# Kernel tuning notes

Measured on AMD Instinct MI355X. Metric: run time of the kernel, lower is better.

Reference implementation:

```python
import jax, jax.numpy as jnp
import numpy as np

B, LQ, LK, D = 8, 2048, 2048, 128
NEG = -100000.0


def setup_inputs() -> dict:
    key = jax.random.key(0)
    kq, kk, kv, km = jax.random.split(key, 4)
    q = jax.random.normal(kq, (B, LQ, D), dtype=jnp.float32)
    k = jax.random.normal(kk, (B, LK, D), dtype=jnp.float32)
    v = jax.random.normal(kv, (B, LK, D), dtype=jnp.float32)
    mask = jax.random.randint(km, (B, LQ, LK), 0, 2, dtype=jnp.int32)
    return {"q": q, "k": k, "v": v, "mask": mask}


def reference(q, k, v, mask):
    # atten_score = q @ k^T / sqrt(d)   [B, Lq, Lk]
    scores = jnp.einsum("bqd,bkd->bqk", q, k) / jnp.sqrt(jnp.float32(q.shape[-1]))
    # mask_mod == 2: additive mask, masked positions pushed to large negative
    scores = scores + mask.astype(jnp.float32) * NEG
    # sigmoid instead of softmax (no normalization across keys)
    attn = jax.nn.sigmoid(scores)
    return jnp.einsum("bqk,bkd->bqd", attn, v)
```

## Files before the change

kernel.cpp:

```cpp
#include <hip/hip_runtime.h>
#include <hip/hip_bf16.h>

#define B_   8
#define LQ_  2048
#define LK_  2048
#define D_   128
#define QBLK 64
#define KBLK 64
#define NT   (LK_ / KBLK)
#define THREADS 512
#define SCALE 0.08838834764831845f

typedef __attribute__((ext_vector_type(8))) __bf16 bf16x8;
typedef __attribute__((ext_vector_type(4))) __bf16 bf16x4;
typedef __attribute__((ext_vector_type(4))) float  f32x4;
typedef __attribute__((ext_vector_type(4))) float  fx4;

#define QS_OFF 0
#define KS_OFF 8704
#define VT_OFF 17408
#define PS_OFF 26624
#define SMEM_ELEMS 31744

__global__ __launch_bounds__(THREADS, 2)
void sigattn_kernel(const float* __restrict__ q, const float* __restrict__ k,
                    const float* __restrict__ v, const int* __restrict__ mask,
                    float* __restrict__ out)
{
    __shared__ __bf16 smem[SMEM_ELEMS];

    const int tid  = threadIdx.x;
    const int lane = tid & 63;
    const int wid  = tid >> 6;
    const int qg   = wid & 3;
    const int kg   = wid >> 2;
    const int l15  = lane & 15;
    const int g    = lane >> 4;

    const int bid   = blockIdx.x;
    const int b     = bid & 7;
    const int q0    = (bid >> 3) * QBLK;

    const float* qb = q + (size_t)b * LQ_ * D_ + (size_t)q0 * D_;
    const float* kb = k + (size_t)b * LK_ * D_;
    const float* vb = v + (size_t)b * LK_ * D_;
    const int*   mb = mask + (size_t)b * LQ_ * LK_ + (size_t)q0 * LK_;
    float*       ob = out + (size_t)b * LQ_ * D_ + (size_t)q0 * D_;

    __bf16* Qs = smem + QS_OFF;
    __bf16* Ks = smem + KS_OFF;
    __bf16* Vt = smem + VT_OFF;
    __bf16* Ps = smem + PS_OFF + wid * 640;

    const int dv  = tid & 127;
    const int kq8 = tid >> 7;

    int mcur[8];

#pragma unroll
    for (int i = 0; i < 4; ++i) {
        int idx = tid + i * THREADS;
        int row = idx >> 5, c4 = idx & 31;
        fx4 f = *(const fx4*)(qb + row * D_ + c4 * 4);
        bf16x4 w; w[0]=(__bf16)f[0]; w[1]=(__bf16)f[1]; w[2]=(__bf16)f[2]; w[3]=(__bf16)f[3];
        *(bf16x4*)(Qs + row * 136 + c4 * 4) = w;
    }
#pragma unroll
    for (int i = 0; i < 4; ++i) {
        int idx = tid + i * THREADS;
        int row = idx >> 5, c4 = idx & 31;
        fx4 f = *(const fx4*)(kb + row * D_ + c4 * 4);
        bf16x4 w; w[0]=(__bf16)f[0]; w[1]=(__bf16)f[1]; w[2]=(__bf16)f[2]; w[3]=(__bf16)f[3];
        *(bf16x4*)(Ks + row * 136 + c4 * 4) = w;
    }
#pragma unroll
    for (int i = 0; i < 4; ++i) {
        int quad = kq8 + i * 4;
        bf16x4 w;
#pragma unroll
        for (int j = 0; j < 4; ++j) w[j] = (__bf16)vb[(quad * 4 + j) * D_ + dv];
        *(bf16x4*)(Vt + dv * 72 + quad * 4) = w;
    }
#pragma unroll
    for (int n2 = 0; n2 < 2; ++n2)
#pragma unroll
        for (int r = 0; r < 4; ++r)
            mcur[n2 * 4 + r] = mb[(qg * 16 + 4 * g + r) * LK_ + (kg * 32 + n2 * 16 + l15)];

    __syncthreads();

    bf16x8 qfrag[4];
#pragma unroll
    for (int dblk = 0; dblk < 4; ++dblk)
        qfrag[dblk] = *(const bf16x8*)(Qs + (qg * 16 + l15) * 136 + dblk * 32 + g * 8);

    f32x4 oacc[8];
#pragma unroll
    for (int nb = 0; nb < 8; ++nb) oacc[nb] = (f32x4){0.f, 0.f, 0.f, 0.f};

    for (int t = 0; t < NT; ++t) {
        const bool more = (t + 1 < NT);

        fx4   kreg[4];
        float vreg[16];
        int   mnxt[8];
        if (more) {
            const int kt = (t + 1) * KBLK;
#pragma unroll
            for (int i = 0; i < 4; ++i) {
                int idx = tid + i * THREADS;
                int row = idx >> 5, c4 = idx & 31;
                kreg[i] = *(const fx4*)(kb + (kt + row) * D_ + c4 * 4);
            }
#pragma unroll
            for (int i = 0; i < 4; ++i) {
                int quad = kq8 + i * 4;
#pragma unroll
                for (int j = 0; j < 4; ++j)
                    vreg[i * 4 + j] = vb[(kt + quad * 4 + j) * D_ + dv];
            }
#pragma unroll
            for (int n2 = 0; n2 < 2; ++n2)
#pragma unroll
                for (int r = 0; r < 4; ++r)
                    mnxt[n2 * 4 + r] = mb[(qg * 16 + 4 * g + r) * LK_ + (kt + kg * 32 + n2 * 16 + l15)];
        }

        f32x4 sacc[2];
        sacc[0] = (f32x4){0.f, 0.f, 0.f, 0.f};
        sacc[1] = (f32x4){0.f, 0.f, 0.f, 0.f};
#pragma unroll
        for (int n2 = 0; n2 < 2; ++n2) {
            const __bf16* krow = Ks + (kg * 32 + n2 * 16 + l15) * 136 + g * 8;
#pragma unroll
            for (int dblk = 0; dblk < 4; ++dblk) {
                bf16x8 bfr = *(const bf16x8*)(krow + dblk * 32);
                sacc[n2] = __builtin_amdgcn_mfma_f32_16x16x32_bf16(qfrag[dblk], bfr, sacc[n2], 0, 0, 0);
            }
        }

#pragma unroll
        for (int n2 = 0; n2 < 2; ++n2)
#pragma unroll
            for (int r = 0; r < 4; ++r) {
                float s = sacc[n2][r] * SCALE;
                float p = (mcur[n2 * 4 + r] != 0) ? 0.0f : 1.0f / (1.0f + __expf(-s));
                Ps[(4 * g + r) * 40 + n2 * 16 + l15] = (__bf16)p;
            }

        bf16x8 pfrag = *(const bf16x8*)(Ps + l15 * 40 + g * 8);
#pragma unroll
        for (int nb = 0; nb < 8; ++nb) {
            bf16x8 vfr = *(const bf16x8*)(Vt + (nb * 16 + l15) * 72 + kg * 32 + g * 8);
            oacc[nb] = __builtin_amdgcn_mfma_f32_16x16x32_bf16(pfrag, vfr, oacc[nb], 0, 0, 0);
        }

        __syncthreads();

        if (more) {
#pragma unroll
            for (int i = 0; i < 4; ++i) {
                int idx = tid + i * THREADS;
                int row = idx >> 5, c4 = idx & 31;
                bf16x4 w;
                w[0]=(__bf16)kreg[i][0]; w[1]=(__bf16)kreg[i][1];
                w[2]=(__bf16)kreg[i][2]; w[3]=(__bf16)kreg[i][3];
                *(bf16x4*)(Ks + row * 136 + c4 * 4) = w;
            }
#pragma unroll
            for (int i = 0; i < 4; ++i) {
                int quad = kq8 + i * 4;
                bf16x4 w;
#pragma unroll
                for (int j = 0; j < 4; ++j) w[j] = (__bf16)vreg[i * 4 + j];
                *(bf16x4*)(Vt + dv * 72 + quad * 4) = w;
            }
#pragma unroll
            for (int j = 0; j < 8; ++j) mcur[j] = mnxt[j];
        }

        __syncthreads();
    }

    float* red = (float*)smem;
    if (kg == 0) {
#pragma unroll
        for (int nb = 0; nb < 8; ++nb)
#pragma unroll
            for (int r = 0; r < 4; ++r)
                red[(qg * 16 + 4 * g + r) * 132 + nb * 16 + l15] = oacc[nb][r];
    }
    __syncthreads();
    if (kg == 1) {
#pragma unroll
        for (int nb = 0; nb < 8; ++nb)
#pragma unroll
            for (int r = 0; r < 4; ++r) {
                int row = qg * 16 + 4 * g + r;
                float val = red[row * 132 + nb * 16 + l15] + oacc[nb][r];
                ob[(size_t)row * D_ + nb * 16 + l15] = val;
            }
    }
}

extern "C" void kernel_launch(void* const* d_in, const int* in_sizes, int n_in,
                              void* d_out, int out_size, void* d_ws, size_t ws_size,
                              hipStream_t stream) {
    const float* q    = (const float*)d_in[0];
    const float* k    = (const float*)d_in[1];
    const float* v    = (const float*)d_in[2];
    const int*   mask = (const int*)d_in[3];
    float*       out  = (float*)d_out;

    dim3 grid(B_ * (LQ_ / QBLK));
    dim3 block(THREADS);
    sigattn_kernel<<<grid, block, 0, stream>>>(q, k, v, mask, out);
}
```

Baseline: 237.6 us.

## Precast K/V to bf16 in prep kernels and stream fragments directly from global

Adds two pre-kernels that convert K to bf16 and transpose V to bf16 in a permuted layout in the workspace. The main kernel now loads its MFMA fragments straight from global memory (L2-resident) instead of staging through LDS, which removes the per-tile barriers. Warps are regrouped into 2 query groups × 2 key slices × 2 key-tile parities, each warp covering 32 query rows. The mask is read with vectorized nontemporal loads, and the sigmoid uses exp2 plus a hardware reciprocal. The cost is two extra launches, more redundant global and L2 traffic per warp, and a four-stage serialized reduction at the end.

```diff
diff --git a/kernel.cpp b/kernel.cpp
--- a/kernel.cpp
+++ b/kernel.cpp
@@ -7,199 +7,220 @@
 #define D_   128
 #define QBLK 64
 #define KBLK 64
-#define NT   (LK_ / KBLK)
 #define THREADS 512
 #define SCALE 0.08838834764831845f
+#define NEGL2E (-1.44269504088896340736f * SCALE)
 
 typedef __attribute__((ext_vector_type(8))) __bf16 bf16x8;
-typedef __attribute__((ext_vector_type(4))) __bf16 bf16x4;
 typedef __attribute__((ext_vector_type(4))) float  f32x4;
 typedef __attribute__((ext_vector_type(4))) float  fx4;
-
-#define QS_OFF 0
-#define KS_OFF 8704
-#define VT_OFF 17408
-#define PS_OFF 26624
-#define SMEM_ELEMS 31744
+typedef __attribute__((ext_vector_type(4))) int    i32x4;
+
+__global__ __launch_bounds__(256)
+void kprep(const float* __restrict__ k, __bf16* __restrict__ kb)
+{
+    size_t i = ((size_t)blockIdx.x * 256 + threadIdx.x) * 8;
+    fx4 a = *(const fx4*)(k + i);
+    fx4 b = *(const fx4*)(k + i + 4);
+    bf16x8 w;
+#pragma unroll
+    for (int j = 0; j < 4; ++j) { w[j] = (__bf16)a[j]; w[4 + j] = (__bf16)b[j]; }
+    *(bf16x8*)(kb + i) = w;
+}
+
+__global__ __launch_bounds__(128)
+void vprep(const float* __restrict__ v, __bf16* __restrict__ vt)
+{
+    const int b  = blockIdx.x & 7;
+    const int k0 = (blockIdx.x >> 3) * 64;
+    const int d  = threadIdx.x;
+    const float* vb = v + ((size_t)b * LK_ + k0) * D_ + d;
+    __bf16* vr = vt + ((size_t)b * D_ + d) * LK_ + k0;
+#pragma unroll
+    for (int grp = 0; grp < 2; ++grp) {
+#pragma unroll
+        for (int g = 0; g < 4; ++g) {
+            bf16x8 w;
+#pragma unroll
+            for (int e = 0; e < 8; ++e) {
+                int h = e >> 2, j = e & 3;
+                int key = grp * 32 + h * 16 + g * 4 + j;
+                w[e] = (__bf16)vb[(size_t)key * D_];
+            }
+            *(bf16x8*)(vr + grp * 32 + g * 8) = w;
+        }
+    }
+}
 
 __global__ __launch_bounds__(THREADS, 2)
-void sigattn_kernel(const float* __restrict__ q, const float* __restrict__ k,
-                    const float* __restrict__ v, const int* __restrict__ mask,
-                    float* __restrict__ out)
+void sigattn_main(const float* __restrict__ q, const int* __restrict__ mask,
+                  const __bf16* __restrict__ Kb, const __bf16* __restrict__ Vt,
+                  float* __restrict__ out)
 {
-    __shared__ __bf16 smem[SMEM_ELEMS];
+    __shared__ float red[64 * 132];
 
     const int tid  = threadIdx.x;
     const int lane = tid & 63;
-    const int wid  = tid >> 6;
-    const int qg   = wid & 3;
-    const int kg   = wid >> 2;
     const int l15  = lane & 15;
     const int g    = lane >> 4;
+    const int wid  = tid >> 6;
+    const int qg   = wid & 1;
+    const int kg   = (wid >> 1) & 1;
+    const int tp   = wid >> 2;
 
     const int bid   = blockIdx.x;
     const int b     = bid & 7;
     const int q0    = (bid >> 3) * QBLK;
-
-    const float* qb = q + (size_t)b * LQ_ * D_ + (size_t)q0 * D_;
-    const float* kb = k + (size_t)b * LK_ * D_;
-    const float* vb = v + (size_t)b * LK_ * D_;
-    const int*   mb = mask + (size_t)b * LQ_ * LK_ + (size_t)q0 * LK_;
-    float*       ob = out + (size_t)b * LQ_ * D_ + (size_t)q0 * D_;
-
-    __bf16* Qs = smem + QS_OFF;
-    __bf16* Ks = smem + KS_OFF;
-    __bf16* Vt = smem + VT_OFF;
-    __bf16* Ps = smem + PS_OFF + wid * 640;
-
-    const int dv  = tid & 127;
-    const int kq8 = tid >> 7;
-
-    int mcur[8];
-
-#pragma unroll
-    for (int i = 0; i < 4; ++i) {
-        int idx = tid + i * THREADS;
+    const int qbase = qg * 32;
+
+    const float*  qb = q    + ((size_t)b * LQ_ + q0) * D_;
+    const int*    mb = mask + ((size_t)b * LQ_ + q0) * LK_;
+    const __bf16* kb = Kb   + (size_t)b * LK_ * D_;
+    const __bf16* vt = Vt   + (size_t)b * D_ * LK_;
+    float*        ob = out  + ((size_t)b * LQ_ + q0) * D_;
+
+    bf16x8 qfrag[2][4];
+#pragma unroll
+    for (int qq = 0; qq < 2; ++qq) {
+        const float* qrow = qb + (size_t)(qbase + qq * 16 + l15) * D_;
+#pragma unroll
+        for (int dblk = 0; dblk < 4; ++dblk) {
+            fx4 f0 = *(const fx4*)(qrow + dblk * 32 + g * 8);
+            fx4 f1 = *(const fx4*)(qrow + dblk * 32 + g * 8 + 4);
+            bf16x8 w;
+#pragma unroll
+            for (int j = 0; j < 4; ++j) { w[j] = (__bf16)f0[j]; w[4 + j] = (__bf16)f1[j]; }
+            qfrag[qq][dblk] = w;
+        }
+    }
+
+    f32x4 oacc[2][8];
+#pragma unroll
+    for (int qq = 0; qq < 2; ++qq)
+#pragma unroll
+        for (int nb = 0; nb < 8; ++nb) oacc[qq][nb] = (f32x4){0.f, 0.f, 0.f, 0.f};
+
+    const int* mr[2];
+    mr[0] = mb + (size_t)(qbase + l15) * LK_ + kg * 32 + 4 * g;
+    mr[1] = mr[0] + (size_t)16 * LK_;
+
+    int kt = tp * KBLK;
+    i32x4 mcur[2][2];
+#pragma unroll
+    for (int qq = 0; qq < 2; ++qq)
+#pragma unroll
+        for (int ksl = 0; ksl < 2; ++ksl)
+            mcur[qq][ksl] = __builtin_nontemporal_load((const i32x4*)(mr[qq] + kt + ksl * 16));
+
+    for (int i = 0; i < 16; ++i, kt += 2 * KBLK) {
+        const int ktp = (i < 15) ? kt + 2 * KBLK : kt;
+
+        i32x4 mnxt[2][2];
+#pragma unroll
+        for (int qq = 0; qq < 2; ++qq)
+#pragma unroll
+            for (int ksl = 0; ksl < 2; ++ksl)
+                mnxt[qq][ksl] = __builtin_nontemporal_load((const i32x4*)(mr[qq] + ktp + ksl * 16));
+
+        bf16x8 kfr[2][4];
+#pragma unroll
+        for (int ksl = 0; ksl < 2; ++ksl)
+#pragma unroll
+            for (int dblk = 0; dblk < 4; ++dblk)
+                kfr[ksl][dblk] = *(const bf16x8*)(kb + (size_t)(kt + kg * 32 + ksl * 16 + l15) * D_ + dblk * 32 + g * 8);
+
+        bf16x8 vfr[8];
+#pragma unroll
+        for (int nb = 0; nb < 8; ++nb)
+            vfr[nb] = *(const bf16x8*)(vt + (size_t)(nb * 16 + l15) * LK_ + kt + kg * 32 + g * 8);
+
+        f32x4 sacc[2][2];
+#pragma unroll
+        for (int qq = 0; qq < 2; ++qq)
+#pragma unroll
+            for (int ksl = 0; ksl < 2; ++ksl)
+                sacc[qq][ksl] = (f32x4){0.f, 0.f, 0.f, 0.f};
+#pragma unroll
+        for (int ksl = 0; ksl < 2; ++ksl)
+#pragma unroll
+            for (int dblk = 0; dblk < 4; ++dblk) {
+                bf16x8 a = kfr[ksl][dblk];
+#pragma unroll
+                for (int qq = 0; qq < 2; ++qq)
+                    sacc[qq][ksl] = __builtin_amdgcn_mfma_f32_16x16x32_bf16(a, qfrag[qq][dblk], sacc[qq][ksl], 0, 0, 0);
+            }
+
+        bf16x8 pfrag[2];
+#pragma unroll
+        for (int qq = 0; qq < 2; ++qq)
+#pragma unroll
+            for (int ksl = 0; ksl < 2; ++ksl)
+#pragma unroll
+                for (int r = 0; r < 4; ++r) {
+                    float e = exp2f(sacc[qq][ksl][r] * NEGL2E);
+                    float p = __builtin_amdgcn_rcpf(1.0f + e);
+                    p = (mcur[qq][ksl][r] != 0) ? 0.0f : p;
+                    pfrag[qq][ksl * 4 + r] = (__bf16)p;
+                }
+
+#pragma unroll
+        for (int nb = 0; nb < 8; ++nb)
+#pragma unroll
+            for (int qq = 0; qq < 2; ++qq)
+                oacc[qq][nb] = __builtin_amdgcn_mfma_f32_16x16x32_bf16(pfrag[qq], vfr[nb], oacc[qq][nb], 0, 0, 0);
+
+#pragma unroll
+        for (int qq = 0; qq < 2; ++qq)
+#pragma unroll
+            for (int ksl = 0; ksl < 2; ++ksl) mcur[qq][ksl] = mnxt[qq][ksl];
+    }
+
+    if (tp == 0 && kg == 0) {
+#pragma unroll
+        for (int qq = 0; qq < 2; ++qq)
+#pragma unroll
+            for (int nb = 0; nb < 8; ++nb)
+#pragma unroll
+                for (int r = 0; r < 4; ++r)
+                    red[(qbase + qq * 16 + 4 * g + r) * 132 + nb * 16 + l15] = oacc[qq][nb][r];
+    }
+    __syncthreads();
+    if (tp == 0 && kg == 1) {
+#pragma unroll
+        for (int qq = 0; qq < 2; ++qq)
+#pragma unroll
+            for (int nb = 0; nb < 8; ++nb)
+#pragma unroll
+                for (int r = 0; r < 4; ++r)
+                    red[(qbase + qq * 16 + 4 * g + r) * 132 + nb * 16 + l15] += oacc[qq][nb][r];
+    }
+    __syncthreads();
+    if (tp == 1 && kg == 0) {
+#pragma unroll
+        for (int qq = 0; qq < 2; ++qq)
+#pragma unroll
+            for (int nb = 0; nb < 8; ++nb)
+#pragma unroll
+                for (int r = 0; r < 4; ++r)
+                    red[(qbase + qq * 16 + 4 * g + r) * 132 + nb * 16 + l15] += oacc[qq][nb][r];
+    }
+    __syncthreads();
+    if (tp == 1 && kg == 1) {
+#pragma unroll
+        for (int qq = 0; qq < 2; ++qq)
+#pragma unroll
+            for (int nb = 0; nb < 8; ++nb)
+#pragma unroll
+                for (int r = 0; r < 4; ++r)
+                    red[(qbase + qq * 16 + 4 * g + r) * 132 + nb * 16 + l15] += oacc[qq][nb][r];
+    }
+    __syncthreads();
+#pragma unroll
+    for (int i2 = 0; i2 < 4; ++i2) {
+        int idx = tid + i2 * THREADS;
         int row = idx >> 5, c4 = idx & 31;
-        fx4 f = *(const fx4*)(qb + row * D_ + c4 * 4);
-        bf16x4 w; w[0]=(__bf16)f[0]; w[1]=(__bf16)f[1]; w[2]=(__bf16)f[2]; w[3]=(__bf16)f[3];
-        *(bf16x4*)(Qs + row * 136 + c4 * 4) = w;
-    }
-#pragma unroll
-    for (int i = 0; i < 4; ++i) {
-        int idx = tid + i * THREADS;
-        int row = idx >> 5, c4 = idx & 31;
-        fx4 f = *(const fx4*)(kb + row * D_ + c4 * 4);
-        bf16x4 w; w[0]=(__bf16)f[0]; w[1]=(__bf16)f[1]; w[2]=(__bf16)f[2]; w[3]=(__bf16)f[3];
-        *(bf16x4*)(Ks + row * 136 + c4 * 4) = w;
-    }
-#pragma unroll
-    for (int i = 0; i < 4; ++i) {
-        int quad = kq8 + i * 4;
-        bf16x4 w;
-#pragma unroll
-        for (int j = 0; j < 4; ++j) w[j] = (__bf16)vb[(quad * 4 + j) * D_ + dv];
-        *(bf16x4*)(Vt + dv * 72 + quad * 4) = w;
-    }
-#pragma unroll
-    for (int n2 = 0; n2 < 2; ++n2)
-#pragma unroll
-        for (int r = 0; r < 4; ++r)
-            mcur[n2 * 4 + r] = mb[(qg * 16 + 4 * g + r) * LK_ + (kg * 32 + n2 * 16 + l15)];
-
-    __syncthreads();
-
-    bf16x8 qfrag[4];
-#pragma unroll
-    for (int dblk = 0; dblk < 4; ++dblk)
-        qfrag[dblk] = *(const bf16x8*)(Qs + (qg * 16 + l15) * 136 + dblk * 32 + g * 8);
-
-    f32x4 oacc[8];
-#pragma unroll
-    for (int nb = 0; nb < 8; ++nb) oacc[nb] = (f32x4){0.f, 0.f, 0.f, 0.f};
-
-    for (int t = 0; t < NT; ++t) {
-        const bool more = (t + 1 < NT);
-
-        fx4   kreg[4];
-        float vreg[16];
-        int   mnxt[8];
-        if (more) {
-            const int kt = (t + 1) * KBLK;
-#pragma unroll
-            for (int i = 0; i < 4; ++i) {
-                int idx = tid + i * THREADS;
-                int row = idx >> 5, c4 = idx & 31;
-                kreg[i] = *(const fx4*)(kb + (kt + row) * D_ + c4 * 4);
-            }
-#pragma unroll
-            for (int i = 0; i < 4; ++i) {
-                int quad = kq8 + i * 4;
-#pragma unroll
-                for (int j = 0; j < 4; ++j)
-                    vreg[i * 4 + j] = vb[(kt + quad * 4 + j) * D_ + dv];
-            }
-#pragma unroll
-            for (int n2 = 0; n2 < 2; ++n2)
-#pragma unroll
-                for (int r = 0; r < 4; ++r)
-                    mnxt[n2 * 4 + r] = mb[(qg * 16 + 4 * g + r) * LK_ + (kt + kg * 32 + n2 * 16 + l15)];
-        }
-
-        f32x4 sacc[2];
-        sacc[0] = (f32x4){0.f, 0.f, 0.f, 0.f};
-        sacc[1] = (f32x4){0.f, 0.f, 0.f, 0.f};
-#pragma unroll
-        for (int n2 = 0; n2 < 2; ++n2) {
-            const __bf16* krow = Ks + (kg * 32 + n2 * 16 + l15) * 136 + g * 8;
-#pragma unroll
-            for (int dblk = 0; dblk < 4; ++dblk) {
-                bf16x8 bfr = *(const bf16x8*)(krow + dblk * 32);
-                sacc[n2] = __builtin_amdgcn_mfma_f32_16x16x32_bf16(qfrag[dblk], bfr, sacc[n2], 0, 0, 0);
-            }
-        }
-
-#pragma unroll
-        for (int n2 = 0; n2 < 2; ++n2)
-#pragma unroll
-            for (int r = 0; r < 4; ++r) {
-                float s = sacc[n2][r] * SCALE;
-                float p = (mcur[n2 * 4 + r] != 0) ? 0.0f : 1.0f / (1.0f + __expf(-s));
-                Ps[(4 * g + r) * 40 + n2 * 16 + l15] = (__bf16)p;
-            }
-
-        bf16x8 pfrag = *(const bf16x8*)(Ps + l15 * 40 + g * 8);
-#pragma unroll
-        for (int nb = 0; nb < 8; ++nb) {
-            bf16x8 vfr = *(const bf16x8*)(Vt + (nb * 16 + l15) * 72 + kg * 32 + g * 8);
-            oacc[nb] = __builtin_amdgcn_mfma_f32_16x16x32_bf16(pfrag, vfr, oacc[nb], 0, 0, 0);
-        }
-
-        __syncthreads();
-
-        if (more) {
-#pragma unroll
-            for (int i = 0; i < 4; ++i) {
-                int idx = tid + i * THREADS;
-                int row = idx >> 5, c4 = idx & 31;
-                bf16x4 w;
-                w[0]=(__bf16)kreg[i][0]; w[1]=(__bf16)kreg[i][1];
-                w[2]=(__bf16)kreg[i][2]; w[3]=(__bf16)kreg[i][3];
-                *(bf16x4*)(Ks + row * 136 + c4 * 4) = w;
-            }
-#pragma unroll
-            for (int i = 0; i < 4; ++i) {
-                int quad = kq8 + i * 4;
-                bf16x4 w;
-#pragma unroll
-                for (int j = 0; j < 4; ++j) w[j] = (__bf16)vreg[i * 4 + j];
-                *(bf16x4*)(Vt + dv * 72 + quad * 4) = w;
-            }
-#pragma unroll
-            for (int j = 0; j < 8; ++j) mcur[j] = mnxt[j];
-        }
-
-        __syncthreads();
-    }
-
-    float* red = (float*)smem;
-    if (kg == 0) {
-#pragma unroll
-        for (int nb = 0; nb < 8; ++nb)
-#pragma unroll
-            for (int r = 0; r < 4; ++r)
-                red[(qg * 16 + 4 * g + r) * 132 + nb * 16 + l15] = oacc[nb][r];
-    }
-    __syncthreads();
-    if (kg == 1) {
-#pragma unroll
-        for (int nb = 0; nb < 8; ++nb)
-#pragma unroll
-            for (int r = 0; r < 4; ++r) {
-                int row = qg * 16 + 4 * g + r;
-                float val = red[row * 132 + nb * 16 + l15] + oacc[nb][r];
-                ob[(size_t)row * D_ + nb * 16 + l15] = val;
-            }
+        fx4 val = *(const fx4*)(red + row * 132 + c4 * 4);
+        __builtin_nontemporal_store(val, (fx4*)(ob + (size_t)row * D_ + c4 * 4));
     }
 }
 
@@ -212,7 +233,10 @@
     const int*   mask = (const int*)d_in[3];
     float*       out  = (float*)d_out;
 
-    dim3 grid(B_ * (LQ_ / QBLK));
-    dim3 block(THREADS);
-    sigattn_kernel<<<grid, block, 0, stream>>>(q, k, v, mask, out);
-}
+    __bf16* Kb = (__bf16*)d_ws;
+    __bf16* Vt = (__bf16*)d_ws + (size_t)2097152;
+
+    kprep<<<dim3(1024), dim3(256), 0, stream>>>(k, Kb);
+    vprep<<<dim3(256), dim3(128), 0, stream>>>(v, Vt);
+    sigattn_main<<<dim3(256), dim3(THREADS), 0, stream>>>(q, mask, Kb, Vt, out);
+}
```

Measured after the change: 271.6 us. +14.3%, slower.
